# Optimization experiments

Hardware: AMD Instinct MI355X
Metric: run time of the kernel (lower is better)

The kernel has to match this reference:

```python
import jax, jax.numpy as jnp
import numpy as np

R = 16
ALPHA = 16.0
SCALING = ALPHA / R  # = 1.0


def setup_inputs() -> dict:
    key = jax.random.key(0)
    k1, k2, k3 = jax.random.split(key, 3)
    x = jax.random.normal(k1, (4, 4096, 4096), dtype=jnp.float32)
    A = jax.random.normal(k2, (4096, R), dtype=jnp.float32)
    B = jax.random.normal(k3, (R, 4096), dtype=jnp.float32)
    return {"x": x, "A": A, "B": B}


def reference(x, A, B):
    # Faithful to torch: W_delta = A @ B * scaling; out = x @ W_delta
    # (dropout_p=0.0 so dropout is a no-op)
    W_delta = (A @ B) * SCALING  # [in, out]
    return jnp.matmul(x, W_delta)  # [b, s, out]
```

## Files before the change

### kernel.cpp

```cpp
#include <hip/hip_runtime.h>

constexpr int RANK = 16;
constexpr int K = 4096;
constexpr int N = 4096;
constexpr int M = 4 * 4096;
constexpr int KC = 512;
constexpr int NCHUNK = K / KC;
constexpr int ROWS2 = 32;


__global__ __launch_bounds__(256) void lora_xa(const float* __restrict__ x,
                                               const float* __restrict__ A,
                                               float* __restrict__ T) {
  const int lane = threadIdx.x & 63;
  const int tid = threadIdx.x;
  const int wave = tid >> 6;
  const int r0 = blockIdx.x * 16 + wave * 4;

  __shared__ float AsT[RANK][KC];

  const float4* __restrict__ A4 = reinterpret_cast<const float4*>(A);
  const float4* __restrict__ x4 = reinterpret_cast<const float4*>(x);

  float vals[64];
#pragma unroll
  for (int i = 0; i < 64; ++i) vals[i] = 0.0f;

  for (int c = 0; c < NCHUNK; ++c) {
    __syncthreads();
#pragma unroll
    for (int q = 0; q < 8; ++q) {
      const int n = q * 256 + tid;
      const int k = n >> 2;
      const int s = n & 3;
      const float4 v = A4[(size_t)c * 2048 + n];
      AsT[4 * s + 0][k] = v.x;
      AsT[4 * s + 1][k] = v.y;
      AsT[4 * s + 2][k] = v.z;
      AsT[4 * s + 3][k] = v.w;
    }
    __syncthreads();

#pragma unroll
    for (int kbi = 0; kbi < KC / 256; ++kbi) {
      const int klq = kbi * 64 + lane;
      const size_t kgq = (size_t)c * (KC / 4) + klq;

      float4 xv[4];
#pragma unroll
      for (int r = 0; r < 4; ++r)
        xv[r] = x4[(size_t)(r0 + r) * (K / 4) + kgq];

#pragma unroll
      for (int jg = 0; jg < 4; ++jg) {
        float4 a[4];
#pragma unroll
        for (int jj = 0; jj < 4; ++jj)
          a[jj] = *reinterpret_cast<const float4*>(&AsT[4 * jg + jj][klq * 4]);
#pragma unroll
        for (int r = 0; r < 4; ++r) {
#pragma unroll
          for (int jj = 0; jj < 4; ++jj) {
            float acc = vals[r * 16 + 4 * jg + jj];
            acc = fmaf(xv[r].x, a[jj].x, acc);
            acc = fmaf(xv[r].y, a[jj].y, acc);
            acc = fmaf(xv[r].z, a[jj].z, acc);
            acc = fmaf(xv[r].w, a[jj].w, acc);
            vals[r * 16 + 4 * jg + jj] = acc;
          }
        }
      }
    }
  }

#define RSTEP(HALF)                                            \
  {                                                            \
    const bool hi = (lane & (HALF)) != 0;                      \
    _Pragma("unroll")                                          \
    for (int i = 0; i < (HALF); ++i) {                         \
      const float send = hi ? vals[i] : vals[i + (HALF)];      \
      const float keep = hi ? vals[i + (HALF)] : vals[i];      \
      vals[i] = keep + __shfl_xor(send, (HALF), 64);           \
    }                                                          \
  }
  RSTEP(32)
  RSTEP(16)
  RSTEP(8)
  RSTEP(4)
  RSTEP(2)
  RSTEP(1)
#undef RSTEP

  T[(size_t)(r0 + (lane >> 4)) * RANK + (lane & 15)] = vals[0];
}

__global__ __launch_bounds__(256) void lora_tb(const float* __restrict__ T,
                                               const float* __restrict__ B,
                                               float* __restrict__ out) {
  const int n0 = blockIdx.x * 1024 + threadIdx.x * 4;
  const int r0 = blockIdx.y * ROWS2;

  const float4* __restrict__ B4 = reinterpret_cast<const float4*>(B);
  float4* __restrict__ out4 = reinterpret_cast<float4*>(out);

  float4 b[16];
#pragma unroll
  for (int j = 0; j < RANK; ++j) b[j] = B4[((size_t)j * N + n0) >> 2];

  for (int r = 0; r < ROWS2; ++r) {
    const float* __restrict__ t = T + (size_t)(r0 + r) * RANK;
    float4 acc;
    acc.x = acc.y = acc.z = acc.w = 0.0f;
#pragma unroll
    for (int j = 0; j < RANK; ++j) {
      const float ts = t[j];
      acc.x = fmaf(ts, b[j].x, acc.x);
      acc.y = fmaf(ts, b[j].y, acc.y);
      acc.z = fmaf(ts, b[j].z, acc.z);
      acc.w = fmaf(ts, b[j].w, acc.w);
    }
    out4[((size_t)(r0 + r) * N + n0) >> 2] = acc;
  }
}

extern "C" void kernel_launch(void* const* d_in, const int* in_sizes, int n_in,
                              void* d_out, int out_size, void* d_ws, size_t ws_size,
                              hipStream_t stream) {
  const float* x = (const float*)d_in[0];
  const float* A = (const float*)d_in[1];
  const float* B = (const float*)d_in[2];
  float* out = (float*)d_out;
  float* T = (float*)d_ws;

  lora_xa<<<M / 16, 256, 0, stream>>>(x, A, T);

  lora_tb<<<dim3(N / 1024, M / ROWS2), 256, 0, stream>>>(T, B, out);
}
```

Measured before the change: 155.4 us.

## Split x@A over K partitions with swizzled LDS and reduce partials in second kernel

The x@A kernel now splits K into four 1024-wide partitions across a second grid dimension. Each block loads its A slice into LDS once, removing the per-chunk reload and its barriers, and uses 512 threads covering 32 rows. The LDS layout is XOR-swizzled to cut bank conflicts on the transposed stores. Partial T results go to workspace and are summed in the T@B kernel, which adds extra partial reads and needs a larger workspace.

New measurement: 162.5 us. 4.6% more time.

```diff
diff --git a/kernel.cpp b/kernel.cpp
--- a/kernel.cpp
+++ b/kernel.cpp
@@ -4,70 +4,71 @@
 constexpr int K = 4096;
 constexpr int N = 4096;
 constexpr int M = 4 * 4096;
-constexpr int KC = 512;
-constexpr int NCHUNK = K / KC;
+constexpr int KQ = 1024;
+constexpr int NPART = K / KQ;
+constexpr int ROWSB = 32;
 constexpr int ROWS2 = 32;
 
 
-__global__ __launch_bounds__(256) void lora_xa(const float* __restrict__ x,
-                                               const float* __restrict__ A,
-                                               float* __restrict__ T) {
-  const int lane = threadIdx.x & 63;
+__global__ __launch_bounds__(512, 4) void lora_xa(const float* __restrict__ x,
+                                                  const float* __restrict__ A,
+                                                  float* __restrict__ Tp) {
   const int tid = threadIdx.x;
+  const int lane = tid & 63;
   const int wave = tid >> 6;
-  const int r0 = blockIdx.x * 16 + wave * 4;
+  const int r0 = blockIdx.x * ROWSB + wave * 4;
+  const int part = blockIdx.y;
 
-  __shared__ float AsT[RANK][KC];
+  __shared__ float AsT[RANK][KQ];
+  float4* __restrict__ AsT4 = reinterpret_cast<float4*>(&AsT[0][0]);
 
   const float4* __restrict__ A4 = reinterpret_cast<const float4*>(A);
   const float4* __restrict__ x4 = reinterpret_cast<const float4*>(x);
+
+#pragma unroll
+  for (int q = 0; q < 8; ++q) {
+    const int n = q * 512 + tid;
+    const int k = n >> 2;
+    const int s = n & 3;
+    const float4 v = A4[(size_t)part * 4096 + n];
+    AsT[4 * s + 0][k ^ (((4 * s + 0) & 7) << 2)] = v.x;
+    AsT[4 * s + 1][k ^ (((4 * s + 1) & 7) << 2)] = v.y;
+    AsT[4 * s + 2][k ^ (((4 * s + 2) & 7) << 2)] = v.z;
+    AsT[4 * s + 3][k ^ (((4 * s + 3) & 7) << 2)] = v.w;
+  }
+  __syncthreads();
 
   float vals[64];
 #pragma unroll
   for (int i = 0; i < 64; ++i) vals[i] = 0.0f;
 
-  for (int c = 0; c < NCHUNK; ++c) {
-    __syncthreads();
 #pragma unroll
-    for (int q = 0; q < 8; ++q) {
-      const int n = q * 256 + tid;
-      const int k = n >> 2;
-      const int s = n & 3;
-      const float4 v = A4[(size_t)c * 2048 + n];
-      AsT[4 * s + 0][k] = v.x;
-      AsT[4 * s + 1][k] = v.y;
-      AsT[4 * s + 2][k] = v.z;
-      AsT[4 * s + 3][k] = v.w;
-    }
-    __syncthreads();
+  for (int step = 0; step < KQ / 256; ++step) {
+    const int q4 = step * 64 + lane;
+
+    float4 xv[4];
+#pragma unroll
+    for (int r = 0; r < 4; ++r)
+      xv[r] = x4[(size_t)(r0 + r) * (K / 4) + part * (KQ / 4) + q4];
 
 #pragma unroll
-    for (int kbi = 0; kbi < KC / 256; ++kbi) {
-      const int klq = kbi * 64 + lane;
-      const size_t kgq = (size_t)c * (KC / 4) + klq;
-
-      float4 xv[4];
+    for (int jg = 0; jg < 4; ++jg) {
+      float4 a[4];
 #pragma unroll
-      for (int r = 0; r < 4; ++r)
-        xv[r] = x4[(size_t)(r0 + r) * (K / 4) + kgq];
-
+      for (int jj = 0; jj < 4; ++jj) {
+        const int j = 4 * jg + jj;
+        a[jj] = AsT4[j * (KQ / 4) + (q4 ^ (j & 7))];
+      }
 #pragma unroll
-      for (int jg = 0; jg < 4; ++jg) {
-        float4 a[4];
+      for (int r = 0; r < 4; ++r) {
 #pragma unroll
-        for (int jj = 0; jj < 4; ++jj)
-          a[jj] = *reinterpret_cast<const float4*>(&AsT[4 * jg + jj][klq * 4]);
-#pragma unroll
-        for (int r = 0; r < 4; ++r) {
-#pragma unroll
-          for (int jj = 0; jj < 4; ++jj) {
-            float acc = vals[r * 16 + 4 * jg + jj];
-            acc = fmaf(xv[r].x, a[jj].x, acc);
-            acc = fmaf(xv[r].y, a[jj].y, acc);
-            acc = fmaf(xv[r].z, a[jj].z, acc);
-            acc = fmaf(xv[r].w, a[jj].w, acc);
-            vals[r * 16 + 4 * jg + jj] = acc;
-          }
+        for (int jj = 0; jj < 4; ++jj) {
+          float acc = vals[r * 16 + 4 * jg + jj];
+          acc = fmaf(xv[r].x, a[jj].x, acc);
+          acc = fmaf(xv[r].y, a[jj].y, acc);
+          acc = fmaf(xv[r].z, a[jj].z, acc);
+          acc = fmaf(xv[r].w, a[jj].w, acc);
+          vals[r * 16 + 4 * jg + jj] = acc;
         }
       }
     }
@@ -91,16 +92,18 @@
   RSTEP(1)
 #undef RSTEP
 
-  T[(size_t)(r0 + (lane >> 4)) * RANK + (lane & 15)] = vals[0];
+  Tp[(size_t)part * (M * RANK) + (size_t)(r0 + (lane >> 4)) * RANK + (lane & 15)] =
+      vals[0];
 }
 
-__global__ __launch_bounds__(256) void lora_tb(const float* __restrict__ T,
+__global__ __launch_bounds__(256) void lora_tb(const float* __restrict__ Tp,
                                                const float* __restrict__ B,
                                                float* __restrict__ out) {
   const int n0 = blockIdx.x * 1024 + threadIdx.x * 4;
   const int r0 = blockIdx.y * ROWS2;
 
   const float4* __restrict__ B4 = reinterpret_cast<const float4*>(B);
+  const float4* __restrict__ Tq = reinterpret_cast<const float4*>(Tp);
   float4* __restrict__ out4 = reinterpret_cast<float4*>(out);
 
   float4 b[16];
@@ -108,16 +111,32 @@
   for (int j = 0; j < RANK; ++j) b[j] = B4[((size_t)j * N + n0) >> 2];
 
   for (int r = 0; r < ROWS2; ++r) {
-    const float* __restrict__ t = T + (size_t)(r0 + r) * RANK;
+    float4 t[4];
+#pragma unroll
+    for (int jg = 0; jg < 4; ++jg) {
+      float4 acc = Tq[((size_t)0 * M + (r0 + r)) * 4 + jg];
+#pragma unroll
+      for (int p = 1; p < NPART; ++p) {
+        const float4 v = Tq[((size_t)p * M + (r0 + r)) * 4 + jg];
+        acc.x += v.x; acc.y += v.y; acc.z += v.z; acc.w += v.w;
+      }
+      t[jg] = acc;
+    }
+
     float4 acc;
     acc.x = acc.y = acc.z = acc.w = 0.0f;
 #pragma unroll
-    for (int j = 0; j < RANK; ++j) {
-      const float ts = t[j];
-      acc.x = fmaf(ts, b[j].x, acc.x);
-      acc.y = fmaf(ts, b[j].y, acc.y);
-      acc.z = fmaf(ts, b[j].z, acc.z);
-      acc.w = fmaf(ts, b[j].w, acc.w);
+    for (int jg = 0; jg < 4; ++jg) {
+#pragma unroll
+      for (int jj = 0; jj < 4; ++jj) {
+        const int j = 4 * jg + jj;
+        const float ts = (jj == 0) ? t[jg].x : (jj == 1) ? t[jg].y
+                        : (jj == 2) ? t[jg].z : t[jg].w;
+        acc.x = fmaf(ts, b[j].x, acc.x);
+        acc.y = fmaf(ts, b[j].y, acc.y);
+        acc.z = fmaf(ts, b[j].z, acc.z);
+        acc.w = fmaf(ts, b[j].w, acc.w);
+      }
     }
     out4[((size_t)(r0 + r) * N + n0) >> 2] = acc;
   }
@@ -130,9 +149,9 @@
   const float* A = (const float*)d_in[1];
   const float* B = (const float*)d_in[2];
   float* out = (float*)d_out;
-  float* T = (float*)d_ws;
+  float* Tp = (float*)d_ws;
 
-  lora_xa<<<M / 16, 256, 0, stream>>>(x, A, T);
+  lora_xa<<<dim3(M / ROWSB, NPART), 512, 0, stream>>>(x, A, Tp);
 
-  lora_tb<<<dim3(N / 1024, M / ROWS2), 256, 0, stream>>>(T, B, out);
+  lora_tb<<<dim3(N / 1024, M / ROWS2), 256, 0, stream>>>(Tp, B, out);
 }
```
